# Optimization experiments

Hardware: AMD Instinct MI355X
Metric: run time of the kernel (lower is better)

The kernel has to match this reference:

```python
import jax, jax.numpy as jnp
import numpy as np

BATCH, IN_F, OUT_F = 1024, 512, 512
GRID_SIZE, SPLINE_ORDER = 32, 3
P_DEACTIVATE = 0.1


def b_splines(x, grid, k):
    """x: (n, in), grid: (in, G+2k+1) -> bases (n, in, G+k). Cox-de Boor recursion."""
    x = x[..., None]  # (n, in, 1)
    bases = ((x >= grid[:, :-1]) & (x < grid[:, 1:])).astype(x.dtype)
    for j in range(1, k + 1):
        left = (x - grid[:, : -(j + 1)]) / (grid[:, j:-1] - grid[:, : -(j + 1)])
        right = (grid[:, j + 1:] - x) / (grid[:, j + 1:] - grid[:, 1:-j])
        bases = left * bases[..., :-1] + right * bases[..., 1:]
    return bases


def setup_inputs() -> dict:
    key = jax.random.key(0)
    k1, k2, k3, k4, k5 = jax.random.split(key, 5)
    # uniform extended grid over [-1, 1], same for every input feature
    h = 2.0 / GRID_SIZE
    knots = np.arange(-SPLINE_ORDER, GRID_SIZE + SPLINE_ORDER + 1, dtype=np.float32) * h - 1.0
    grid = jnp.asarray(np.tile(knots, (IN_F, 1)))  # (in, G+2k+1)
    return {
        "x": jax.random.normal(k1, (BATCH, IN_F), jnp.float32),
        "base_weight": jax.random.normal(k2, (OUT_F, IN_F), jnp.float32) * 0.05,
        "spline_weight": jax.random.normal(k3, (OUT_F, IN_F, GRID_SIZE + SPLINE_ORDER), jnp.float32) * 0.1,
        "spline_scaler": jax.random.normal(k4, (OUT_F, IN_F), jnp.float32),
        "grid": grid,
        "deactivate_mask": jax.random.bernoulli(k5, P_DEACTIVATE, (OUT_F, IN_F)),
    }


def reference(x, base_weight, spline_weight, spline_scaler, grid, deactivate_mask):
    k = SPLINE_ORDER
    weights = spline_weight * spline_scaler[..., None]  # scaled_spline_weight (o, i, c)
    # base path: F.linear(silu(x), base_weight)
    base_out = jax.nn.silu(x) @ base_weight.T  # (b, o)
    # spline path
    bases = b_splines(x, grid, k)  # (b, i, c)
    contrib = jnp.einsum('bic,oic->boi', bases, weights)  # (b, o, i)
    # linear fallback from spline values at grid endpoints
    gmin = grid[:, k].min()
    gmax = grid[:, -k - 1].max()
    ends_x = jnp.stack([gmin, gmax])[:, None] * jnp.ones((1, x.shape[1]), x.dtype)  # (2, i)
    y_ends = jnp.einsum('nic,oic->noi', b_splines(ends_x, grid, k), weights)  # (2, o, i)
    y_start, y_end = y_ends[0], y_ends[1]
    dx = gmax - gmin
    degenerate = jnp.abs(dx) < 1e-8
    a = jnp.where(degenerate, 0.0, (y_end - y_start) / jnp.where(degenerate, 1.0, dx))  # (o, i)
    b = y_start - a * gmin
    lin = a[None] * x[:, None, :] + b[None]  # (b, o, i)
    final = jnp.where(deactivate_mask[None], lin, contrib)
    return base_out + final.sum(axis=2)
```

## Files before the change

### kernel.cpp

```cpp
#include <hip/hip_runtime.h>
#include <hip/hip_bf16.h>


typedef unsigned short u16;
typedef unsigned int u32;
typedef unsigned long long u64;
typedef __attribute__((ext_vector_type(8))) short short8;
typedef __attribute__((ext_vector_type(4))) float floatx4;

#define IN_F 512
#define OUT_F 512
#define BATCH 1024
#define K_SPLINE (IN_F * 36)
#define K_BASE_OFF K_SPLINE
#define K_LIN_OFF (K_SPLINE + IN_F)
#define K_TOT (K_SPLINE + 2 * IN_F)
#define SPLITS 32
#define MN (BATCH * OUT_F)

static __device__ inline u16 f2b(float f) {
  union { float f; u32 u; } v; v.f = f;
  u32 r = v.u + 0x7FFFu + ((v.u >> 16) & 1u);
  return (u16)(r >> 16);
}
static __device__ inline float b2f(u32 lo16) {
  union { u32 u; float f; } v; v.u = lo16 << 16; return v.f;
}

__global__ __launch_bounds__(256) void prep_kernel(
    const float* __restrict__ bw, const float* __restrict__ sw,
    const float* __restrict__ sc, const void* __restrict__ maskp,
    const float* __restrict__ x, u16* __restrict__ B,
    float* __restrict__ bias_part, u16* __restrict__ A) {
  __shared__ __align__(16) u64 lds64[1120 * 4];
  __shared__ int sflag;
  __shared__ float ws4[4];
  int blk = blockIdx.x, t = threadIdx.x;

  if (blk >= 1024) {
    int bix = blk - 1024;
    int b = bix >> 1;
    int i0 = (bix & 1) << 8;
    int i = i0 + t;
    float xv = x[(size_t)b * IN_F + i];

    u64* myrow = lds64 + t * 9;
#pragma unroll
    for (int j = 0; j < 9; ++j) myrow[j] = 0;

    int mc = (int)floorf((xv + 1.1875f) * 16.0f);
    float gm = (float)mc * 0.0625f - 1.1875f;
    if (xv < gm) { mc -= 1; gm -= 0.0625f; }
    else if (xv >= gm + 0.0625f) { mc += 1; gm += 0.0625f; }
    if (mc >= 0 && mc <= 37) {
      float t_ = (xv - gm) * 16.0f;
      float t2 = t_ * t_, t3 = t2 * t_;
      float omt = 1.0f - t_;
      u16 r0 = f2b(omt * omt * omt * (1.0f / 6.0f));
      u16 r1 = f2b((3.0f * t3 - 6.0f * t2 + 4.0f) * (1.0f / 6.0f));
      u16 r2 = f2b((-3.0f * t3 + 3.0f * t2 + 3.0f * t_ + 1.0f) * (1.0f / 6.0f));
      float f0 = b2f(r0), f1 = b2f(r1), f2 = b2f(r2);
      u16 bv[4] = {r0, r1, r2, f2b(1.0f - f0 - f1 - f2)};
      u16* lds_u = (u16*)lds64;
#pragma unroll
      for (int j = 0; j < 4; ++j) {
        int c = mc - 3 + j;
        if ((u32)c < 35u) lds_u[t * 36 + c] = bv[j];
      }
    }
    __syncthreads();

    u64* dstA = (u64*)(A + (size_t)b * K_TOT + (size_t)i0 * 36);
#pragma unroll
    for (int j = 0; j < 9; ++j) dstA[j * 256 + t] = lds64[j * 256 + t];

    float sl = xv / (1.0f + __expf(-xv));
    A[(size_t)b * K_TOT + K_BASE_OFF + i] = f2b(sl);
    A[(size_t)b * K_TOT + K_LIN_OFF + i] = f2b(xv);
    return;
  }

  float* lds_f = (float*)lds64;
  int id = blk * 256 + t;
  int o = id >> 9, i = id & 511;
  int i0 = (blk & 1) * 256;

  const float* swb = sw + ((size_t)o * 512 + i0) * 35;
  const floatx4* sw4 = (const floatx4*)swb;
  floatx4* lds4 = (floatx4*)lds_f;
#pragma unroll
  for (int j = 0; j < 8; ++j) lds4[j * 256 + t] = sw4[j * 256 + t];
  if (t < 192) lds4[8 * 256 + t] = sw4[8 * 256 + t];

  const u32* mw = (const u32*)maskp;
  if (t == 0) sflag = 0;
  __syncthreads();
  if (t < 64) {
    u32 w2 = mw[blk * 64 + t];
    if ((w2 & 0xFFFFFF00u) && w2 != 0x3F800000u) atomicOr(&sflag, 1);
  }
  __syncthreads();
  int fl = sflag;
  if (!(fl & 1)) {
    u32 w1 = mw[blk * 256 + t];
    if (w1 == 0x3F800000u) atomicOr(&sflag, 2);
  }
  __syncthreads();
  fl = sflag;
  bool mk;
  if (fl & 1)      mk = ((const unsigned char*)maskp)[id] != 0;
  else if (fl & 2) mk = ((const float*)maskp)[id] != 0.0f;
  else             mk = ((const int*)maskp)[id] != 0;

  float s = sc[id];
  float w[35];
#pragma unroll
  for (int c = 0; c < 35; ++c) w[c] = lds_f[t * 35 + c] * s;
  __syncthreads();

  float ys = (w[0] + 4.0f * w[1] + w[2]) * (1.0f / 6.0f);
  float ye = (w[32] + 4.0f * w[33] + w[34]) * (1.0f / 6.0f);
  float a = (ye - ys) * 0.5f;
  float bl = ys + a;

  union { u16 r16[36]; u64 r64[9]; } ur;
#pragma unroll
  for (int c = 0; c < 35; ++c) ur.r16[c] = f2b(mk ? 0.0f : w[c]);
  ur.r16[35] = 0;
  u64* myrow = lds64 + t * 9;
#pragma unroll
  for (int j = 0; j < 9; ++j) myrow[j] = ur.r64[j];

  B[(size_t)o * K_TOT + K_BASE_OFF + i] = f2b(bw[id]);
  B[(size_t)o * K_TOT + K_LIN_OFF + i] = f2b(mk ? a : 0.0f);

  float v = mk ? bl : 0.0f;
#pragma unroll
  for (int off = 32; off >= 1; off >>= 1) v += __shfl_down(v, off);
  if ((t & 63) == 0) ws4[t >> 6] = v;
  __syncthreads();
  if (t == 0) bias_part[blk] = ws4[0] + ws4[1] + ws4[2] + ws4[3];

  u64* dst = (u64*)(B + (size_t)o * K_TOT + (size_t)i0 * 36);
#pragma unroll
  for (int j = 0; j < 9; ++j) dst[j * 256 + t] = lds64[j * 256 + t];
}

__global__ __launch_bounds__(512, 4) void gemm_fused(const u16* __restrict__ A,
                                                     const u16* __restrict__ Bp,
                                                     u16* __restrict__ P) {
  __shared__ u16 As[256 * 64];
  __shared__ u16 Bs[128 * 64];

  int t = threadIdx.x;
  int p = blockIdx.x;
  int x_ = p & 7, j = p >> 3;
  int bm = j & 3, idx = j >> 2;
  int bn = x_ & 3;
  int ks = 2 * idx + (x_ >> 2);
  int tile = (bm << 2) | bn;

  int w = t >> 6, l = t & 63;
  int wm = w & 3, wn = w >> 2;

  floatx4 acc[4][4];
#pragma unroll
  for (int pp = 0; pp < 4; ++pp)
#pragma unroll
    for (int q = 0; q < 4; ++q) acc[pp][q] = (floatx4)0.0f;

  int nit = (ks < 16) ? 10 : 9;
  int k0s = (ks < 16) ? ks * 640 : 10240 + (ks - 16) * 576;

  int ra = t >> 3;
  int cg = (t & 7) ^ (ra & 7);
  const u16* Agp = A + (size_t)(bm * 256 + ra) * K_TOT + k0s + cg * 8;
  const u16* Bgp = Bp + (size_t)(bn * 128 + ra) * K_TOT + k0s + cg * 8;
  u16* Asp = As + t * 8;
  u16* Bsp = Bs + t * 8;

  int mr = l & 15;
  int cq = l >> 4;

  for (int kk = 0; kk < nit; ++kk) {
#pragma unroll
    for (int q = 0; q < 4; ++q)
      __builtin_amdgcn_global_load_lds(
          (const __attribute__((address_space(1))) void*)(Agp + (size_t)q * 64 * K_TOT),
          (__attribute__((address_space(3))) void*)(Asp + q * 4096), 16, 0, 0);
#pragma unroll
    for (int q = 0; q < 2; ++q)
      __builtin_amdgcn_global_load_lds(
          (const __attribute__((address_space(1))) void*)(Bgp + (size_t)q * 64 * K_TOT),
          (__attribute__((address_space(3))) void*)(Bsp + q * 4096), 16, 0, 0);
    Agp += 64;
    Bgp += 64;
    __syncthreads();

#pragma unroll
    for (int h = 0; h < 2; ++h) {
      short8 af[4], bf[4];
      int c = h * 4 + cq;
#pragma unroll
      for (int tm = 0; tm < 4; ++tm) {
        int row = wm * 64 + tm * 16 + mr;
        af[tm] = *(const short8*)&As[row * 64 + ((c ^ (row & 7)) << 3)];
      }
#pragma unroll
      for (int tn = 0; tn < 4; ++tn) {
        int row = wn * 64 + tn * 16 + mr;
        bf[tn] = *(const short8*)&Bs[row * 64 + ((c ^ (row & 7)) << 3)];
      }
#pragma unroll
      for (int tm = 0; tm < 4; ++tm)
#pragma unroll
        for (int tn = 0; tn < 4; ++tn)
          acc[tm][tn] = __builtin_amdgcn_mfma_f32_16x16x32_bf16(af[tm], bf[tn], acc[tm][tn], 0, 0, 0);
    }
    __syncthreads();
  }

  u16* Pb = P + ((size_t)tile * SPLITS + ks) * 32768;
#pragma unroll
  for (int q = 0; q < 8; ++q) {
    int tm = q >> 1, tn0 = (q & 1) * 2;
    u16 r[8];
#pragma unroll
    for (int z = 0; z < 4; ++z) r[z] = f2b(acc[tm][tn0][z]);
#pragma unroll
    for (int z = 0; z < 4; ++z) r[4 + z] = f2b(acc[tm][tn0 + 1][z]);
    *(short8*)(Pb + q * 4096 + t * 8) = *(short8*)r;
  }
}

__global__ __launch_bounds__(256) void reduce_kernel(const u16* __restrict__ P,
                                                     const float* __restrict__ bias_part,
                                                     float* __restrict__ out) {
  int rid = blockIdx.x * 256 + threadIdx.x;
  int tile = rid >> 12;
  int rem = rid & 4095;
  int q = rem >> 9, t = rem & 511;
  const u16* base = P + (size_t)tile * SPLITS * 32768 + q * 4096 + t * 8;

  float s[8] = {0, 0, 0, 0, 0, 0, 0, 0};
#pragma unroll
  for (int ks = 0; ks < SPLITS; ++ks) {
    short8 v = *(const short8*)(base + (size_t)ks * 32768);
#pragma unroll
    for (int j = 0; j < 8; ++j) s[j] += b2f((u32)(u16)v[j]);
  }

  int w = t >> 6, l = t & 63;
  int wm = w & 3, wn = w >> 2;
  int bm = tile >> 2, bn = tile & 3;
  int row0 = bm * 256 + wm * 64 + ((l >> 4) << 2);
  int col0 = bn * 128 + wn * 64 + (l & 15);
  int tm = q >> 1, tn0 = (q & 1) * 2;
#pragma unroll
  for (int j = 0; j < 8; ++j) {
    int tn = tn0 + (j >> 2), rr = j & 3;
    int row = row0 + tm * 16 + rr;
    int col = col0 + tn * 16;
    float bsv = bias_part[2 * col] + bias_part[2 * col + 1];
    out[(size_t)row * OUT_F + col] = s[j] + bsv;
  }
}

extern "C" void kernel_launch(void* const* d_in, const int* in_sizes, int n_in,
                              void* d_out, int out_size, void* d_ws, size_t ws_size,
                              hipStream_t stream) {
  const float* x  = (const float*)d_in[0];
  const float* bw = (const float*)d_in[1];
  const float* sw = (const float*)d_in[2];
  const float* sc = (const float*)d_in[3];
  const void* mask = d_in[5];

  const size_t B_BYTES = (size_t)OUT_F * K_TOT * 2;
  const size_t BIAS_OFF = B_BYTES;
  const size_t A_OFF = B_BYTES + 8192;
  const size_t A_BYTES = (size_t)BATCH * K_TOT * 2;
  const size_t P_OFF = A_OFF + A_BYTES;

  char* wsb = (char*)d_ws;
  u16* Bpack = (u16*)wsb;
  float* bias_part = (float*)(wsb + BIAS_OFF);
  u16* Adense = (u16*)(wsb + A_OFF);
  u16* P = (u16*)(wsb + P_OFF);

  prep_kernel<<<3072, 256, 0, stream>>>(bw, sw, sc, mask, x, Bpack, bias_part, Adense);
  gemm_fused<<<512, 512, 0, stream>>>(Adense, Bpack, P);
  reduce_kernel<<<256, 256, 0, stream>>>(P, bias_part, (float*)d_out);
}
```

Measured before the change: 136.2 us.

## Double-buffer LDS in split-K GEMM and halve the K split count

The GEMM kernel now uses two LDS buffers for the A and B tiles. It issues the next tile's global-to-LDS loads before computing on the current one, using an explicit vmcnt wait and raw barriers. The split-K factor drops from 32 to 16 with a uniform K chunk per block, so the grid halves to 256 blocks and the bf16 partial buffer that the reduce kernel reads shrinks. The trade is double LDS use, with launch bounds lowered to 2 blocks per SM, and only one block per CU, which reduces latency hiding from co-resident blocks.

```diff
diff --git a/kernel.cpp b/kernel.cpp
--- a/kernel.cpp
+++ b/kernel.cpp
@@ -15,7 +15,9 @@
 #define K_BASE_OFF K_SPLINE
 #define K_LIN_OFF (K_SPLINE + IN_F)
 #define K_TOT (K_SPLINE + 2 * IN_F)
-#define SPLITS 32
+#define SPLITS 16
+#define KPS 1216
+#define NIT 19
 #define MN (BATCH * OUT_F)
 
 static __device__ inline u16 f2b(float f) {
@@ -146,19 +148,16 @@
   for (int j = 0; j < 9; ++j) dst[j * 256 + t] = lds64[j * 256 + t];
 }
 
-__global__ __launch_bounds__(512, 4) void gemm_fused(const u16* __restrict__ A,
+__global__ __launch_bounds__(512, 2) void gemm_fused(const u16* __restrict__ A,
                                                      const u16* __restrict__ Bp,
                                                      u16* __restrict__ P) {
-  __shared__ u16 As[256 * 64];
-  __shared__ u16 Bs[128 * 64];
+  __shared__ u16 As[2][256 * 64];
+  __shared__ u16 Bs[2][128 * 64];
 
   int t = threadIdx.x;
   int p = blockIdx.x;
-  int x_ = p & 7, j = p >> 3;
-  int bm = j & 3, idx = j >> 2;
-  int bn = x_ & 3;
-  int ks = 2 * idx + (x_ >> 2);
-  int tile = (bm << 2) | bn;
+  int tile = p & 15, ks = p >> 4;
+  int bm = tile >> 2, bn = tile & 3;
 
   int w = t >> 6, l = t & 63;
   int wm = w & 3, wn = w >> 2;
@@ -169,34 +168,55 @@
 #pragma unroll
     for (int q = 0; q < 4; ++q) acc[pp][q] = (floatx4)0.0f;
 
-  int nit = (ks < 16) ? 10 : 9;
-  int k0s = (ks < 16) ? ks * 640 : 10240 + (ks - 16) * 576;
+  int k0s = ks * KPS;
 
   int ra = t >> 3;
   int cg = (t & 7) ^ (ra & 7);
   const u16* Agp = A + (size_t)(bm * 256 + ra) * K_TOT + k0s + cg * 8;
   const u16* Bgp = Bp + (size_t)(bn * 128 + ra) * K_TOT + k0s + cg * 8;
-  u16* Asp = As + t * 8;
-  u16* Bsp = Bs + t * 8;
 
   int mr = l & 15;
   int cq = l >> 4;
 
-  for (int kk = 0; kk < nit; ++kk) {
-#pragma unroll
-    for (int q = 0; q < 4; ++q)
-      __builtin_amdgcn_global_load_lds(
-          (const __attribute__((address_space(1))) void*)(Agp + (size_t)q * 64 * K_TOT),
-          (__attribute__((address_space(3))) void*)(Asp + q * 4096), 16, 0, 0);
-#pragma unroll
-    for (int q = 0; q < 2; ++q)
-      __builtin_amdgcn_global_load_lds(
-          (const __attribute__((address_space(1))) void*)(Bgp + (size_t)q * 64 * K_TOT),
-          (__attribute__((address_space(3))) void*)(Bsp + q * 4096), 16, 0, 0);
-    Agp += 64;
-    Bgp += 64;
-    __syncthreads();
-
+#define STAGE(buf, koff)                                                       \
+  do {                                                                         \
+    const u16* a_ = Agp + (koff);                                              \
+    const u16* b_ = Bgp + (koff);                                              \
+    __builtin_amdgcn_global_load_lds(                                          \
+        (const __attribute__((address_space(1))) void*)a_,                     \
+        (__attribute__((address_space(3))) void*)(&As[buf][t * 8]), 16, 0, 0); \
+    __builtin_amdgcn_global_load_lds(                                          \
+        (const __attribute__((address_space(1))) void*)(a_ + (size_t)64 * K_TOT),   \
+        (__attribute__((address_space(3))) void*)(&As[buf][4096 + t * 8]), 16, 0, 0);\
+    __builtin_amdgcn_global_load_lds(                                          \
+        (const __attribute__((address_space(1))) void*)(a_ + (size_t)128 * K_TOT),  \
+        (__attribute__((address_space(3))) void*)(&As[buf][8192 + t * 8]), 16, 0, 0);\
+    __builtin_amdgcn_global_load_lds(                                          \
+        (const __attribute__((address_space(1))) void*)(a_ + (size_t)192 * K_TOT),  \
+        (__attribute__((address_space(3))) void*)(&As[buf][12288 + t * 8]), 16, 0, 0);\
+    __builtin_amdgcn_global_load_lds(                                          \
+        (const __attribute__((address_space(1))) void*)b_,                     \
+        (__attribute__((address_space(3))) void*)(&Bs[buf][t * 8]), 16, 0, 0); \
+    __builtin_amdgcn_global_load_lds(                                          \
+        (const __attribute__((address_space(1))) void*)(b_ + (size_t)64 * K_TOT),   \
+        (__attribute__((address_space(3))) void*)(&Bs[buf][4096 + t * 8]), 16, 0, 0);\
+  } while (0)
+
+  STAGE(0, 0);
+
+  for (int kk = 0; kk < NIT; ++kk) {
+    int cur = kk & 1;
+    if (kk + 1 < NIT) {
+      STAGE(cur ^ 1, (kk + 1) * 64);
+      asm volatile("s_waitcnt vmcnt(6)" ::: "memory");
+    } else {
+      asm volatile("s_waitcnt vmcnt(0)" ::: "memory");
+    }
+    __builtin_amdgcn_s_barrier();
+    __builtin_amdgcn_sched_barrier(0);
+
+    const u16* Ac = &As[cur][0];
+    const u16* Bc = &Bs[cur][0];
 #pragma unroll
     for (int h = 0; h < 2; ++h) {
       short8 af[4], bf[4];
@@ -204,12 +224,12 @@
 #pragma unroll
       for (int tm = 0; tm < 4; ++tm) {
         int row = wm * 64 + tm * 16 + mr;
-        af[tm] = *(const short8*)&As[row * 64 + ((c ^ (row & 7)) << 3)];
+        af[tm] = *(const short8*)&Ac[row * 64 + ((c ^ (row & 7)) << 3)];
       }
 #pragma unroll
       for (int tn = 0; tn < 4; ++tn) {
         int row = wn * 64 + tn * 16 + mr;
-        bf[tn] = *(const short8*)&Bs[row * 64 + ((c ^ (row & 7)) << 3)];
+        bf[tn] = *(const short8*)&Bc[row * 64 + ((c ^ (row & 7)) << 3)];
       }
 #pragma unroll
       for (int tm = 0; tm < 4; ++tm)
@@ -217,8 +237,11 @@
         for (int tn = 0; tn < 4; ++tn)
           acc[tm][tn] = __builtin_amdgcn_mfma_f32_16x16x32_bf16(af[tm], bf[tn], acc[tm][tn], 0, 0, 0);
     }
-    __syncthreads();
-  }
+
+    __builtin_amdgcn_s_barrier();
+    __builtin_amdgcn_sched_barrier(0);
+  }
+#undef STAGE
 
   u16* Pb = P + ((size_t)tile * SPLITS + ks) * 32768;
 #pragma unroll
@@ -288,6 +311,6 @@
   u16* P = (u16*)(wsb + P_OFF);
 
   prep_kernel<<<3072, 256, 0, stream>>>(bw, sw, sc, mask, x, Bpack, bias_part, Adense);
-  gemm_fused<<<512, 512, 0, stream>>>(Adense, Bpack, P);
+  gemm_fused<<<256, 512, 0, stream>>>(Adense, Bpack, P);
   reduce_kernel<<<256, 256, 0, stream>>>(P, bias_part, (float*)d_out);
 }
```

Result: no change. 134.5 us (median of 2 runs) (-1.3%).
